# Kernel tuning notes

Hardware: AMD Instinct MI355X
Metric: run time of the kernel (lower is better)

## Reference

```python
import jax, jax.numpy as jnp
import numpy as np

E = 1024
H = 16
HD = E // H


def _shift(pos_score):
    # Transformer-XL relative shift trick. pos_score: [B,H,Q,K]
    B, nH, Q, K = pos_score.shape
    zeros = jnp.zeros((B, nH, Q, 1), pos_score.dtype)
    padded = jnp.concatenate([zeros, pos_score], axis=-1)  # [B,H,Q,K+1]
    padded = padded.reshape(B, nH, K + 1, Q)
    return padded[:, :, 1:].reshape(B, nH, Q, K)


def setup_inputs() -> dict:
    key = jax.random.key(0)
    ks = jax.random.split(key, 14)
    B, S = 2, 1024
    s = 1.0 / np.sqrt(E)
    inp = {
        "query": jax.random.normal(ks[0], (B, S, E), jnp.float32),
        "key": jax.random.normal(ks[1], (B, S, E), jnp.float32),
        "value": jax.random.normal(ks[2], (B, S, E), jnp.float32),
        "pos_embedding": jax.random.normal(ks[3], (B, S, E), jnp.float32),
        "Wq": jax.random.normal(ks[4], (E, E), jnp.float32) * s,
        "bq": jnp.zeros((E,), jnp.float32),
        "Wk": jax.random.normal(ks[5], (E, E), jnp.float32) * s,
        "bk": jnp.zeros((E,), jnp.float32),
        "Wv": jax.random.normal(ks[6], (E, E), jnp.float32) * s,
        "bv": jnp.zeros((E,), jnp.float32),
        "Wp": jax.random.normal(ks[7], (E, E), jnp.float32) * s,
        "U": jax.random.normal(ks[8], (H, HD), jnp.float32) * s,
        "V": jax.random.normal(ks[9], (H, HD), jnp.float32) * s,
        "Wo": jax.random.normal(ks[10], (E, E), jnp.float32) * s,
        "bo": jnp.zeros((E,), jnp.float32),
    }
    return inp


def reference(query, key, value, pos_embedding, Wq, bq, Wk, bk, Wv, bv, Wp, U, V, Wo, bo):
    B, Q, _ = query.shape
    K = key.shape[1]
    d = jnp.asarray(np.sqrt(E), query.dtype)

    q = (query @ Wq + bq).reshape(B, Q, H, HD)
    k = (key @ Wk + bk).reshape(B, K, H, HD)
    v = (value @ Wv + bv).reshape(B, K, H, HD)
    R = (pos_embedding @ Wp).reshape(B, -1, H, HD)

    content_score = jnp.einsum('bqhd,bkhd->bhqk', q + U, k)
    position_score = jnp.einsum('bqhd,bkhd->bhqk', q + V, R)
    position_score = _shift(position_score)
    attention_score = (content_score + position_score) / d  # no softmax in original

    # NOTE: faithful to original einsum 'bhqk,bvhd->bqhd' where k and v are
    # both contracted independently (sums scores over k, values over v).
    alpha = jnp.einsum('bhqk,bvhd->bqhd', attention_score, v).reshape(B, Q, E)
    return alpha @ Wo + bo
```

## Files before the change

kernel.cpp:

```cpp
#include <hip/hip_runtime.h>
#include <cstddef>
#include <cstdint>

#define E_ 1024
#define H_ 16
#define HD_ 64
#define B_ 2
#define S_ 1024
#define NSEG 64
#define SEGLEN (S_/NSEG)
#define CHUNKS 64
#define CHLEN (S_/CHUNKS)
#define SCALE 0.03125f

typedef __attribute__((ext_vector_type(8))) short bf16x8;
typedef __attribute__((ext_vector_type(4))) float f32x4;

__device__ __forceinline__ unsigned short f2bf_rne(float x) {
  uint32_t u = __float_as_uint(x);
  uint32_t r = u + 0x7FFFu + ((u >> 16) & 1u);
  return (unsigned short)(r >> 16);
}
__device__ __forceinline__ float bf2f(unsigned short h) {
  return __uint_as_float(((uint32_t)h) << 16);
}
__device__ __forceinline__ void gload_lds16(const void* g, void* l) {
  __builtin_amdgcn_global_load_lds(
      (const __attribute__((address_space(1))) void*)g,
      (__attribute__((address_space(3))) void*)l, 16, 0, 0);
}

__global__ __launch_bounds__(256) void kP1(
    const float* __restrict__ query, const float* __restrict__ pos,
    const float* __restrict__ key,   const float* __restrict__ value,
    const float* __restrict__ Wq,    const float* __restrict__ Wp,
    float* __restrict__ seg, unsigned short* __restrict__ Aq,
    float* __restrict__ pk, float* __restrict__ pv,
    unsigned short* __restrict__ Btq, unsigned short* __restrict__ Btp) {
  __shared__ float tile[32][33];
  int bid = blockIdx.x;
  int t = threadIdx.x;
  if (bid < 512) {
    int idx = bid*256 + t;
    int e = idx % E_;
    int g = (idx / E_) % NSEG;
    int b = idx / (E_*NSEG);
    const float* p = pos + ((size_t)(b*S_ + g*SEGLEN))*E_ + e;
    float s = 0.f;
    #pragma unroll
    for (int i = 0; i < SEGLEN; ++i) s += p[(size_t)i*E_];
    seg[(b*NSEG + g)*E_ + e] = s;
  } else if (bid < 2560) {
    int idx = (bid-512)*256 + t;
    int e4 = idx & 255;
    int r  = idx >> 8;
    float4 v = ((const float4*)query)[idx];
    float xs[4] = {v.x, v.y, v.z, v.w};
    ushort4 hi, lo;
    unsigned short hb; float lf;
    hb = f2bf_rne(xs[0]); lf = xs[0]-bf2f(hb); hi.x = hb; lo.x = f2bf_rne(lf);
    hb = f2bf_rne(xs[1]); lf = xs[1]-bf2f(hb); hi.y = hb; lo.y = f2bf_rne(lf);
    hb = f2bf_rne(xs[2]); lf = xs[2]-bf2f(hb); hi.z = hb; lo.z = f2bf_rne(lf);
    hb = f2bf_rne(xs[3]); lf = xs[3]-bf2f(hb); hi.w = hb; lo.w = f2bf_rne(lf);
    *(ushort4*)&Aq[(size_t)r*2048 + e4*4]        = hi;
    *(ushort4*)&Aq[(size_t)r*2048 + 1024 + e4*4] = lo;
  } else if (bid < 4608) {
    int f = bid - 2560;
    int nt = f & 31, kt = (f >> 5) & 31, z = f >> 10;
    const float* W = z ? Wp : Wq;
    unsigned short* Bt = z ? Btp : Btq;
    int lr = t >> 3;
    int lc = (t & 7) * 4;
    float4 v = *(const float4*)&W[(size_t)(kt*32 + lr)*E_ + nt*32 + lc];
    tile[lr][lc+0] = v.x; tile[lr][lc+1] = v.y;
    tile[lr][lc+2] = v.z; tile[lr][lc+3] = v.w;
    __syncthreads();
    int n = nt*32 + lr;
    ushort4 hi, lo;
    unsigned short hb; float lf; float x;
    x = tile[lc+0][lr]; hb = f2bf_rne(x); lf = x-bf2f(hb); hi.x = hb; lo.x = f2bf_rne(lf);
    x = tile[lc+1][lr]; hb = f2bf_rne(x); lf = x-bf2f(hb); hi.y = hb; lo.y = f2bf_rne(lf);
    x = tile[lc+2][lr]; hb = f2bf_rne(x); lf = x-bf2f(hb); hi.z = hb; lo.z = f2bf_rne(lf);
    x = tile[lc+3][lr]; hb = f2bf_rne(x); lf = x-bf2f(hb); hi.w = hb; lo.w = f2bf_rne(lf);
    *(ushort4*)&Bt[(size_t)n*2048 + kt*32 + lc]        = hi;
    *(ushort4*)&Bt[(size_t)n*2048 + 1024 + kt*32 + lc] = lo;
  } else {
    int idx = (bid-4608)*256 + t;
    int e = idx % E_;
    int c = (idx / E_) % CHUNKS;
    int b = idx / (E_*CHUNKS);
    const float* kp = key   + ((size_t)(b*S_ + c*CHLEN))*E_ + e;
    const float* vp = value + ((size_t)(b*S_ + c*CHLEN))*E_ + e;
    float sk = 0.f, sv = 0.f;
    #pragma unroll
    for (int s = 0; s < CHLEN; ++s) {
      sk += kp[(size_t)s*E_];
      sv += vp[(size_t)s*E_];
    }
    pk[(b*CHUNKS + c)*E_ + e] = sk;
    pv[(b*CHUNKS + c)*E_ + e] = sv;
  }
}

__global__ __launch_bounds__(256) void kP2(
    const float* __restrict__ pos, const float* __restrict__ seg,
    unsigned short* __restrict__ Ap,
    const float* __restrict__ pk, const float* __restrict__ pv,
    const float* __restrict__ bk, const float* __restrict__ bv,
    float* __restrict__ colsum, float* __restrict__ ksum,
    float* __restrict__ vsum) {
  int bid = blockIdx.x;
  int t = threadIdx.x;
  if (bid < 512) {
    int idx = bid*256 + t;
    int e = idx % E_;
    int g = (idx / E_) % NSEG;
    int b = idx / (E_*NSEG);
    float run = 0.f;
    for (int gp = 0; gp < g; ++gp) run += seg[(b*NSEG + gp)*E_ + e];
    const float* p = pos + ((size_t)(b*S_ + g*SEGLEN))*E_ + e;
    #pragma unroll
    for (int i = 0; i < SEGLEN; ++i) {
      run += p[(size_t)i*E_];
      size_t row = (size_t)(b*S_ + g*SEGLEN + i);
      unsigned short hb = f2bf_rne(run);
      float lf = run - bf2f(hb);
      Ap[row*2048 + e]        = hb;
      Ap[row*2048 + 1024 + e] = f2bf_rne(lf);
    }
  } else {
    int idx = (bid-512)*256 + t;
    int e = idx & 1023;
    int b = (idx >> 10) & 1;
    int j = idx >> 11;
    const float* p = j ? pv : pk;
    float s = 0.f;
    #pragma unroll 8
    for (int c = 0; c < CHUNKS; ++c) s += p[(b*CHUNKS + c)*E_ + e];
    colsum[idx] = s;
    (j ? vsum : ksum)[b*E_ + e] = (float)S_ * (j ? bv : bk)[e];
  }
}

__global__ __launch_bounds__(256) void kP3(
    const float* __restrict__ colsum, const float* __restrict__ Wk,
    const float* __restrict__ Wv, float* __restrict__ ksum,
    float* __restrict__ vsum) {
  int f = blockIdx.x;
  int j     = f >> 6;
  int slice = (f >> 2) & 15;
  int n     = (f & 3)*256 + threadIdx.x;
  const float* W  = j ? Wv : Wk;
  const float* cs = colsum + j*2048;
  float a0 = 0.f, a1 = 0.f;
  int e0 = slice*64;
  #pragma unroll 8
  for (int i = 0; i < 64; ++i) {
    int e = e0 + i;
    float w = W[(size_t)e*E_ + n];
    a0 += cs[e] * w;
    a1 += cs[1024 + e] * w;
  }
  float* out = j ? vsum : ksum;
  atomicAdd(&out[n], a0);
  atomicAdd(&out[E_ + n], a1);
}

#define GNT 48
__global__ __launch_bounds__(256, 2) void kP4(
    const unsigned short* __restrict__ Aq, const unsigned short* __restrict__ Btq,
    const float* __restrict__ bq,
    const unsigned short* __restrict__ Ap, const unsigned short* __restrict__ Btp,
    float* __restrict__ Cq, float* __restrict__ Cp,
    const float* __restrict__ vsum, const float* __restrict__ Wo,
    float* __restrict__ WV) {
  __shared__ __align__(128) char lds[49152];
  int bid = blockIdx.x;
  const int t = threadIdx.x;
  if (bid >= 512) {
    int idx = (bid-512)*256 + t;
    int n = idx % E_;
    int h = (idx / E_) % H_;
    int b = idx / (E_*H_);
    float acc = 0.f;
    #pragma unroll 8
    for (int d = 0; d < HD_; ++d)
      acc += vsum[b*E_ + h*HD_ + d] * Wo[(size_t)(h*HD_ + d)*E_ + n];
    WV[idx] = acc;
    return;
  }
  int wg = bid;
  int newid = (wg & 7)*64 + (wg >> 3);
  int z  = newid >> 8;
  int bm = (newid >> 4) & 15;
  int bn = newid & 15;
  const int lane = t & 63;
  const int wm = (t >> 6) >> 1;
  const int wn = (t >> 6) & 1;

  const unsigned short* A; const unsigned short* Bt;
  const float* bias; float* C;
  if (z == 0) { A = Aq; Bt = Btq; bias = bq;      C = Cq; }
  else        { A = Ap; Bt = Btp; bias = nullptr; C = Cp; }

  const unsigned short* asrc[4];
  const unsigned short* bsrc[2];
  #pragma unroll
  for (int i = 0; i < 4; ++i) {
    int L = i*4096 + t*16;
    int row = L >> 7, bir = L & 127;
    int sw = bir ^ ((row & 7) << 4);
    asrc[i] = A + (size_t)(bm*128 + row)*2048 + (sw >> 1);
  }
  #pragma unroll
  for (int i = 0; i < 2; ++i) {
    int L = i*4096 + t*16;
    int row = L >> 7, bir = L & 127;
    int sw = bir ^ ((row & 7) << 4);
    bsrc[i] = Bt + (size_t)(bn*64 + row)*2048 + (sw >> 1);
  }
  int aoff[2][4], boff[2][2];
  #pragma unroll
  for (int ks = 0; ks < 2; ++ks) {
    int k0b = (ks*32 + (lane >> 4)*8) * 2;
    #pragma unroll
    for (int mi = 0; mi < 4; ++mi) {
      int row = wm*64 + mi*16 + (lane & 15);
      aoff[ks][mi] = row*128 + (k0b ^ ((row & 7) << 4));
    }
    #pragma unroll
    for (int ni = 0; ni < 2; ++ni) {
      int rown = wn*32 + ni*16 + (lane & 15);
      boff[ks][ni] = rown*128 + (k0b ^ ((rown & 7) << 4));
    }
  }

  f32x4 acc[4][2] = {};

  auto stage = [&](int buf, int kt) {
    int ak = (kt < 32) ? kt : kt - 32;
    int bk = (kt < 16) ? kt : kt - 16;
    char* Ab = lds + buf*16384;
    char* Bb = lds + 32768 + buf*8192;
    #pragma unroll
    for (int i = 0; i < 4; ++i)
      gload_lds16(asrc[i] + ak*64, Ab + i*4096 + t*16);
    #pragma unroll
    for (int i = 0; i < 2; ++i)
      gload_lds16(bsrc[i] + bk*64, Bb + i*4096 + t*16);
  };

  stage(0, 0);
  __syncthreads();
  int cur = 0;
  for (int kt = 0; kt < GNT; ++kt) {
    if (kt + 1 < GNT) stage(cur ^ 1, kt + 1);
    const char* Ab = lds + cur*16384;
    const char* Bb = lds + 32768 + cur*8192;
    bf16x8 af[2][4], bf_[2][2];
    #pragma unroll
    for (int ks = 0; ks < 2; ++ks) {
      #pragma unroll
      for (int mi = 0; mi < 4; ++mi)
        af[ks][mi] = *(const bf16x8*)(Ab + aoff[ks][mi]);
      #pragma unroll
      for (int ni = 0; ni < 2; ++ni)
        bf_[ks][ni] = *(const bf16x8*)(Bb + boff[ks][ni]);
    }
    #pragma unroll
    for (int ks = 0; ks < 2; ++ks)
      #pragma unroll
      for (int mi = 0; mi < 4; ++mi)
        #pragma unroll
        for (int ni = 0; ni < 2; ++ni)
          acc[mi][ni] = __builtin_amdgcn_mfma_f32_16x16x32_bf16(
              af[ks][mi], bf_[ks][ni], acc[mi][ni], 0, 0, 0);
    __syncthreads();
    cur ^= 1;
  }

  #pragma unroll
  for (int mi = 0; mi < 4; ++mi) {
    #pragma unroll
    for (int ni = 0; ni < 2; ++ni) {
      int col  = bn*64 + wn*32 + ni*16 + (lane & 15);
      int row0 = bm*128 + wm*64 + mi*16 + (lane >> 4)*4;
      float badd = bias ? bias[col] : 0.f;
      #pragma unroll
      for (int j = 0; j < 4; ++j)
        C[(size_t)(row0 + j)*E_ + col] = acc[mi][ni][j] + badd;
    }
  }
}

__global__ __launch_bounds__(256) void k6_rs(
    const float* __restrict__ qp, const float* __restrict__ Rpre,
    const float* __restrict__ ksum, const float* __restrict__ U,
    const float* __restrict__ V, float* __restrict__ rs) {
  int w    = blockIdx.x*4 + (threadIdx.x >> 6);
  int lane = threadIdx.x & 63;
  int q = w % S_;
  int h = (w / S_) % H_;
  int b = w / (S_*H_);
  int he = h*HD_ + lane;
  float qv0  = qp[((size_t)(b*S_ + q))*E_ + he];
  float u    = U[he], vv = V[he];
  float ks   = ksum[b*E_ + he];
  float rtot = Rpre[((size_t)(b*S_ + (S_-1)))*E_ + he];
  float tail = rtot;
  if (q <= S_-2) tail -= Rpre[((size_t)(b*S_ + (S_-2-q)))*E_ + he];
  float p = (qv0 + u)*ks + (qv0 + vv)*tail;
  if (q <= S_-3) {
    float qv1 = qp[((size_t)(b*S_ + q + 1))*E_ + he];
    float hd  = Rpre[((size_t)(b*S_ + (S_-3-q)))*E_ + he];
    p += (qv1 + vv)*hd;
  }
  #pragma unroll
  for (int off = 32; off >= 1; off >>= 1)
    p += __shfl_xor(p, off);
  if (lane == 0) rs[(b*H_ + h)*S_ + q] = p * SCALE;
}

__global__ __launch_bounds__(256) void k7_out(
    const float* __restrict__ rs, const float* __restrict__ WV,
    const float* __restrict__ bo, float* __restrict__ out) {
  int idx = blockIdx.x*256 + threadIdx.x;
  int n = idx % E_;
  int q = (idx / E_) % S_;
  int b = idx / (E_*S_);
  float acc = bo[n];
  #pragma unroll
  for (int h = 0; h < H_; ++h)
    acc += rs[(b*H_ + h)*S_ + q] * WV[((size_t)(b*H_ + h))*E_ + n];
  out[idx] = acc;
}

extern "C" void kernel_launch(void* const* d_in, const int* in_sizes, int n_in,
                              void* d_out, int out_size, void* d_ws, size_t ws_size,
                              hipStream_t stream) {
  const float* query = (const float*)d_in[0];
  const float* key   = (const float*)d_in[1];
  const float* value = (const float*)d_in[2];
  const float* pos   = (const float*)d_in[3];
  const float* Wq = (const float*)d_in[4];
  const float* bq = (const float*)d_in[5];
  const float* Wk = (const float*)d_in[6];
  const float* bk = (const float*)d_in[7];
  const float* Wv = (const float*)d_in[8];
  const float* bv = (const float*)d_in[9];
  const float* Wp = (const float*)d_in[10];
  const float* U  = (const float*)d_in[11];
  const float* V  = (const float*)d_in[12];
  const float* Wo = (const float*)d_in[13];
  const float* bo = (const float*)d_in[14];
  float* out = (float*)d_out;
  char* wsb = (char*)d_ws;

  unsigned short* Aqs = (unsigned short*)(wsb);
  unsigned short* Aps = (unsigned short*)(wsb + (8ull<<20));
  unsigned short* Btq = (unsigned short*)(wsb + (16ull<<20));
  unsigned short* Btp = (unsigned short*)(wsb + (20ull<<20));
  float* Rpre  = (float*)(wsb + (24ull<<20));
  char*  smallb = wsb + (32ull<<20);
  float* seg   = (float*)(smallb);
  float* pk    = (float*)(smallb + (512ull<<10));
  float* pv    = (float*)(smallb + (1024ull<<10));
  float* ksum  = (float*)(smallb + (1536ull<<10));
  float* vsum  = (float*)(smallb + (1544ull<<10));
  float* WVb   = (float*)(smallb + (1552ull<<10));
  float* rs    = (float*)(smallb + (1680ull<<10));
  float* qproj = out;
  float* colsum = (float*)(smallb + (1808ull<<10));

  hipLaunchKernelGGL(kP1, dim3(5120), dim3(256), 0, stream,
                     query, pos, key, value, Wq, Wp,
                     seg, Aqs, pk, pv, Btq, Btp);
  hipLaunchKernelGGL(kP2, dim3(528), dim3(256), 0, stream,
                     pos, seg, Aps, pk, pv, bk, bv, colsum, ksum, vsum);
  hipLaunchKernelGGL(kP3, dim3(128), dim3(256), 0, stream,
                     colsum, Wk, Wv, ksum, vsum);
  hipLaunchKernelGGL(kP4, dim3(640), dim3(256), 0, stream,
                     Aqs, Btq, bq, Aps, Btp, qproj, Rpre, vsum, Wo, WVb);
  hipLaunchKernelGGL(k6_rs, dim3(B_*H_*S_/4), dim3(256), 0, stream,
                     qproj, Rpre, ksum, U, V, rs);
  hipLaunchKernelGGL(k7_out, dim3(B_*S_*E_/256), dim3(256), 0, stream,
                     rs, WVb, bo, out);
}
```

Before: 191.5 us.

## Drop bf16 hi/lo split for Q and Wp operands and fuse final kernels

```diff
diff --git a/kernel.cpp b/kernel.cpp
--- a/kernel.cpp
+++ b/kernel.cpp
@@ -55,15 +55,10 @@
     int e4 = idx & 255;
     int r  = idx >> 8;
     float4 v = ((const float4*)query)[idx];
-    float xs[4] = {v.x, v.y, v.z, v.w};
-    ushort4 hi, lo;
-    unsigned short hb; float lf;
-    hb = f2bf_rne(xs[0]); lf = xs[0]-bf2f(hb); hi.x = hb; lo.x = f2bf_rne(lf);
-    hb = f2bf_rne(xs[1]); lf = xs[1]-bf2f(hb); hi.y = hb; lo.y = f2bf_rne(lf);
-    hb = f2bf_rne(xs[2]); lf = xs[2]-bf2f(hb); hi.z = hb; lo.z = f2bf_rne(lf);
-    hb = f2bf_rne(xs[3]); lf = xs[3]-bf2f(hb); hi.w = hb; lo.w = f2bf_rne(lf);
-    *(ushort4*)&Aq[(size_t)r*2048 + e4*4]        = hi;
-    *(ushort4*)&Aq[(size_t)r*2048 + 1024 + e4*4] = lo;
+    ushort4 hi;
+    hi.x = f2bf_rne(v.x); hi.y = f2bf_rne(v.y);
+    hi.z = f2bf_rne(v.z); hi.w = f2bf_rne(v.w);
+    *(ushort4*)&Aq[(size_t)r*1024 + e4*4] = hi;
   } else if (bid < 4608) {
     int f = bid - 2560;
     int nt = f & 31, kt = (f >> 5) & 31, z = f >> 10;
@@ -76,14 +71,10 @@
     tile[lr][lc+2] = v.z; tile[lr][lc+3] = v.w;
     __syncthreads();
     int n = nt*32 + lr;
-    ushort4 hi, lo;
-    unsigned short hb; float lf; float x;
-    x = tile[lc+0][lr]; hb = f2bf_rne(x); lf = x-bf2f(hb); hi.x = hb; lo.x = f2bf_rne(lf);
-    x = tile[lc+1][lr]; hb = f2bf_rne(x); lf = x-bf2f(hb); hi.y = hb; lo.y = f2bf_rne(lf);
-    x = tile[lc+2][lr]; hb = f2bf_rne(x); lf = x-bf2f(hb); hi.z = hb; lo.z = f2bf_rne(lf);
-    x = tile[lc+3][lr]; hb = f2bf_rne(x); lf = x-bf2f(hb); hi.w = hb; lo.w = f2bf_rne(lf);
-    *(ushort4*)&Bt[(size_t)n*2048 + kt*32 + lc]        = hi;
-    *(ushort4*)&Bt[(size_t)n*2048 + 1024 + kt*32 + lc] = lo;
+    ushort4 hi;
+    hi.x = f2bf_rne(tile[lc+0][lr]); hi.y = f2bf_rne(tile[lc+1][lr]);
+    hi.z = f2bf_rne(tile[lc+2][lr]); hi.w = f2bf_rne(tile[lc+3][lr]);
+    *(ushort4*)&Bt[(size_t)n*1024 + kt*32 + lc] = hi;
   } else {
     int idx = (bid-4608)*256 + t;
     int e = idx % E_;
@@ -166,7 +157,6 @@
   atomicAdd(&out[E_ + n], a1);
 }
 
-#define GNT 48
 __global__ __launch_bounds__(256, 2) void kP4(
     const unsigned short* __restrict__ Aq, const unsigned short* __restrict__ Btq,
     const float* __restrict__ bq,
@@ -200,8 +190,9 @@
 
   const unsigned short* A; const unsigned short* Bt;
   const float* bias; float* C;
-  if (z == 0) { A = Aq; Bt = Btq; bias = bq;      C = Cq; }
-  else        { A = Ap; Bt = Btp; bias = nullptr; C = Cp; }
+  int alen, ntot;
+  if (z == 0) { A = Aq; Bt = Btq; bias = bq;      C = Cq; alen = 1024; ntot = 16; }
+  else        { A = Ap; Bt = Btp; bias = nullptr; C = Cp; alen = 2048; ntot = 32; }
 
   const unsigned short* asrc[4];
   const unsigned short* bsrc[2];
@@ -210,14 +201,14 @@
     int L = i*4096 + t*16;
     int row = L >> 7, bir = L & 127;
     int sw = bir ^ ((row & 7) << 4);
-    asrc[i] = A + (size_t)(bm*128 + row)*2048 + (sw >> 1);
+    asrc[i] = A + (size_t)(bm*128 + row)*alen + (sw >> 1);
   }
   #pragma unroll
   for (int i = 0; i < 2; ++i) {
     int L = i*4096 + t*16;
     int row = L >> 7, bir = L & 127;
     int sw = bir ^ ((row & 7) << 4);
-    bsrc[i] = Bt + (size_t)(bn*64 + row)*2048 + (sw >> 1);
+    bsrc[i] = Bt + (size_t)(bn*64 + row)*1024 + (sw >> 1);
   }
   int aoff[2][4], boff[2][2];
   #pragma unroll
@@ -238,7 +229,7 @@
   f32x4 acc[4][2] = {};
 
   auto stage = [&](int buf, int kt) {
-    int ak = (kt < 32) ? kt : kt - 32;
+    int ak = kt;
     int bk = (kt < 16) ? kt : kt - 16;
     char* Ab = lds + buf*16384;
     char* Bb = lds + 32768 + buf*8192;
@@ -253,8 +244,8 @@
   stage(0, 0);
   __syncthreads();
   int cur = 0;
-  for (int kt = 0; kt < GNT; ++kt) {
-    if (kt + 1 < GNT) stage(cur ^ 1, kt + 1);
+  for (int kt = 0; kt < ntot; ++kt) {
+    if (kt + 1 < ntot) stage(cur ^ 1, kt + 1);
     const char* Ab = lds + cur*16384;
     const char* Bb = lds + 32768 + cur*8192;
     bf16x8 af[2][4], bf_[2][2];
@@ -293,46 +284,47 @@
   }
 }
 
-__global__ __launch_bounds__(256) void k6_rs(
+__global__ __launch_bounds__(256) void kFin(
     const float* __restrict__ qp, const float* __restrict__ Rpre,
     const float* __restrict__ ksum, const float* __restrict__ U,
-    const float* __restrict__ V, float* __restrict__ rs) {
-  int w    = blockIdx.x*4 + (threadIdx.x >> 6);
-  int lane = threadIdx.x & 63;
-  int q = w % S_;
-  int h = (w / S_) % H_;
-  int b = w / (S_*H_);
-  int he = h*HD_ + lane;
-  float qv0  = qp[((size_t)(b*S_ + q))*E_ + he];
-  float u    = U[he], vv = V[he];
-  float ks   = ksum[b*E_ + he];
-  float rtot = Rpre[((size_t)(b*S_ + (S_-1)))*E_ + he];
-  float tail = rtot;
-  if (q <= S_-2) tail -= Rpre[((size_t)(b*S_ + (S_-2-q)))*E_ + he];
-  float p = (qv0 + u)*ks + (qv0 + vv)*tail;
-  if (q <= S_-3) {
-    float qv1 = qp[((size_t)(b*S_ + q + 1))*E_ + he];
-    float hd  = Rpre[((size_t)(b*S_ + (S_-3-q)))*E_ + he];
-    p += (qv1 + vv)*hd;
-  }
-  #pragma unroll
-  for (int off = 32; off >= 1; off >>= 1)
-    p += __shfl_xor(p, off);
-  if (lane == 0) rs[(b*H_ + h)*S_ + q] = p * SCALE;
-}
-
-__global__ __launch_bounds__(256) void k7_out(
-    const float* __restrict__ rs, const float* __restrict__ WV,
+    const float* __restrict__ V, const float* __restrict__ WV,
     const float* __restrict__ bo, float* __restrict__ out) {
-  int idx = blockIdx.x*256 + threadIdx.x;
-  int n = idx % E_;
-  int q = (idx / E_) % S_;
-  int b = idx / (E_*S_);
-  float acc = bo[n];
-  #pragma unroll
-  for (int h = 0; h < H_; ++h)
-    acc += rs[(b*H_ + h)*S_ + q] * WV[((size_t)(b*H_ + h))*E_ + n];
-  out[idx] = acc;
+  __shared__ float rsL[H_];
+  int bq = blockIdx.x;
+  int b = bq >> 10, q = bq & 1023;
+  int t = threadIdx.x;
+  int w = t >> 6, lane = t & 63;
+  const float* qrow0 = qp + ((size_t)(b*S_ + q))*E_;
+  const float* rt    = Rpre + ((size_t)(b*S_ + (S_-1)))*E_;
+  #pragma unroll
+  for (int i = 0; i < 4; ++i) {
+    int h = w*4 + i;
+    int he = h*HD_ + lane;
+    float qv0 = qrow0[he];
+    float u = U[he], vv = V[he];
+    float ks = ksum[b*E_ + he];
+    float tail = rt[he];
+    if (q <= S_-2) tail -= Rpre[((size_t)(b*S_ + (S_-2-q)))*E_ + he];
+    float p = (qv0 + u)*ks + (qv0 + vv)*tail;
+    if (q <= S_-3) {
+      float qv1 = qrow0[E_ + he];
+      p += (qv1 + vv)*Rpre[((size_t)(b*S_ + (S_-3-q)))*E_ + he];
+    }
+    #pragma unroll
+    for (int off = 32; off >= 1; off >>= 1)
+      p += __shfl_xor(p, off);
+    if (lane == 0) rsL[h] = p * SCALE;
+  }
+  __syncthreads();
+  #pragma unroll
+  for (int i = 0; i < 4; ++i) {
+    int n = i*256 + t;
+    float acc = bo[n];
+    #pragma unroll
+    for (int h = 0; h < H_; ++h)
+      acc += rsL[h] * WV[((size_t)(b*H_ + h))*E_ + n];
+    out[((size_t)(b*S_ + q))*E_ + n] = acc;
+  }
 }
 
 extern "C" void kernel_launch(void* const* d_in, const int* in_sizes, int n_in,
@@ -357,10 +349,11 @@
   char* wsb = (char*)d_ws;
 
   unsigned short* Aqs = (unsigned short*)(wsb);
-  unsigned short* Aps = (unsigned short*)(wsb + (8ull<<20));
-  unsigned short* Btq = (unsigned short*)(wsb + (16ull<<20));
-  unsigned short* Btp = (unsigned short*)(wsb + (20ull<<20));
-  float* Rpre  = (float*)(wsb + (24ull<<20));
+  unsigned short* Aps = (unsigned short*)(wsb + (4ull<<20));
+  unsigned short* Btq = (unsigned short*)(wsb + (12ull<<20));
+  unsigned short* Btp = (unsigned short*)(wsb + (14ull<<20));
+  float* Rpre  = (float*)(wsb + (16ull<<20));
+  float* qproj = (float*)(wsb + (24ull<<20));
   char*  smallb = wsb + (32ull<<20);
   float* seg   = (float*)(smallb);
   float* pk    = (float*)(smallb + (512ull<<10));
@@ -368,9 +361,7 @@
   float* ksum  = (float*)(smallb + (1536ull<<10));
   float* vsum  = (float*)(smallb + (1544ull<<10));
   float* WVb   = (float*)(smallb + (1552ull<<10));
-  float* rs    = (float*)(smallb + (1680ull<<10));
-  float* qproj = out;
-  float* colsum = (float*)(smallb + (1808ull<<10));
+  float* colsum = (float*)(smallb + (1680ull<<10));
 
   hipLaunchKernelGGL(kP1, dim3(5120), dim3(256), 0, stream,
                      query, pos, key, value, Wq, Wp,
@@ -381,8 +372,6 @@
                      colsum, Wk, Wv, ksum, vsum);
   hipLaunchKernelGGL(kP4, dim3(640), dim3(256), 0, stream,
                      Aqs, Btq, bq, Aps, Btp, qproj, Rpre, vsum, Wo, WVb);
-  hipLaunchKernelGGL(k6_rs, dim3(B_*H_*S_/4), dim3(256), 0, stream,
-                     qproj, Rpre, ksum, U, V, rs);
-  hipLaunchKernelGGL(k7_out, dim3(B_*S_*E_/256), dim3(256), 0, stream,
-                     rs, WVb, bo, out);
-}
+  hipLaunchKernelGGL(kFin, dim3(B_*S_), dim3(256), 0, stream,
+                     qproj, Rpre, ksum, U, V, WVb, bo, out);
+}
```

Measured after the change: 176.0 us. 1.09x faster.
